# Kernel optimization log

Measured on AMD Instinct MI355X. Metric: run time of the kernel, lower is better.

The kernel has to match this reference:

```python
import jax, jax.numpy as jnp
import numpy as np

B = 8192          # graphs
A = 1024          # atoms per graph
F = 32            # max fragments per graph
N = B * A
VIRTUAL_IDX = 4   # HPARAMS.get_node_idx('ligand_virtual')


def setup_inputs() -> dict:
    key = jax.random.key(0)
    k1, k2, k3, k4 = jax.random.split(key, 4)
    pos = jax.random.normal(k1, (N, 3), dtype=jnp.float32) * 10.0
    # -1 marks non-ligand atoms (no fragment), as in frag_idx_map semantics
    frag_idx_map = jax.random.randint(k2, (N,), -1, F, dtype=jnp.int32)
    batch_idx = (jnp.arange(N, dtype=jnp.int32) // A).astype(jnp.int32)
    node_entity = jax.random.randint(k3, (N,), 0, 6, dtype=jnp.int32)
    mask = jax.random.bernoulli(k4, 0.95, (N,))
    return {"pos": pos, "frag_idx_map": frag_idx_map, "batch_idx": batch_idx,
            "node_entity": node_entity, "mask": mask,
            "num_graphs": B, "max_frags_per_graph": F}


def reference(pos, frag_idx_map, batch_idx, node_entity, mask,
              num_graphs, max_frags_per_graph):
    """Fused equivalent of get_flat_fragment_index + get_fragment_com.

    Returns (coms [B*F, 3], counts [B*F], flat_frag_idx [N]).
    Rows of coms beyond a graph's actual fragment count are zero-padded.
    """
    Bn = num_graphs
    Fm = max_frags_per_graph
    is_ligand = frag_idx_map >= 0

    # num_frags_per_graph[i] = max(frag_idx in graph i) + 1 (0 if none)
    fmax = jax.ops.segment_max(jnp.where(is_ligand, frag_idx_map, -1),
                               batch_idx, num_segments=Bn)
    nfrag = jnp.maximum(fmax, -1) + 1  # [B]
    offset = jnp.concatenate([jnp.zeros((1,), nfrag.dtype),
                              jnp.cumsum(nfrag)[:-1]])  # [B]

    # flat fragment index in [0, sum(F_i)), -1 for non-ligand atoms
    flat_frag_idx = jnp.where(is_ligand,
                              frag_idx_map + offset[batch_idx],
                              -1)

    # COM excludes virtual nodes and masked dummies
    valid = is_ligand & mask & (node_entity != VIRTUAL_IDX)
    n_seg = Bn * Fm
    seg = jnp.where(valid, flat_frag_idx, n_seg)  # dump invalid into trash segment
    w = valid.astype(pos.dtype)
    sums = jax.ops.segment_sum(pos * w[:, None], seg, num_segments=n_seg + 1)[:-1]
    cnt = jax.ops.segment_sum(w, seg, num_segments=n_seg + 1)[:-1]
    coms = sums / jnp.maximum(cnt, 1.0)[:, None]
    return coms, cnt, flat_frag_idx
```

## Files before the change

### kernel.cpp

```cpp
#include <hip/hip_runtime.h>

#define GA 1024
#define GF 32
#define VIRT 4

typedef _Float16 half8 __attribute__((ext_vector_type(8)));
typedef float f32x4 __attribute__((ext_vector_type(4)));
typedef unsigned int uint4v __attribute__((ext_vector_type(4)));

#define XSTRIDE 2080
#define KOFF    (4 * XSTRIDE)
#define FOFF    (KOFF + GA)
#define LDSSZ   (FOFF + 4 * GF * 4 * 4)

__device__ __forceinline__ unsigned int h2(float a, float b) {
    const unsigned short lo = __builtin_bit_cast(unsigned short, (_Float16)a);
    const unsigned short hi = __builtin_bit_cast(unsigned short, (_Float16)b);
    return (unsigned int)lo | ((unsigned int)hi << 16);
}

__global__ __launch_bounds__(256) void k_graph_acc(
    const float* __restrict__ pos,
    const int*   __restrict__ frag,
    const int*   __restrict__ entity,
    const int*   __restrict__ mask,
    float*       __restrict__ sums_cnt,
    int*         __restrict__ nfrag,
    unsigned*    __restrict__ frag8u)
{
    const int g    = blockIdx.x;
    const int t    = threadIdx.x;
    const int lane = t & 63;
    const int w    = t >> 6;

    __shared__ alignas(16) unsigned char lds[LDSSZ];
    __shared__ int s_wmax[4];

    const int i0 = g * GA + t * 4;
    const int4  f4 = *(const int4*)(frag   + i0);
    const int4  e4 = *(const int4*)(entity + i0);
    const int4  m4 = *(const int4*)(mask   + i0);
    const float4* p4 = (const float4*)(pos + (size_t)3 * i0);
    const float4 pa = p4[0], pb = p4[1], pc = p4[2];

    const unsigned s8p = (f4.x & 0xFFu)         | ((f4.y & 0xFFu) << 8)
                       | ((f4.z & 0xFFu) << 16) | ((unsigned)(f4.w & 0xFFu) << 24);
    frag8u[(size_t)g * (GA / 4) + t] = s8p;

    #define KEY(F,M,E) ((unsigned)(((F) >= 0 && (M) != 0 && (E) != VIRT) ? (unsigned)(F) : 0xFFu))
    const unsigned kp = KEY(f4.x,m4.x,e4.x)        | (KEY(f4.y,m4.y,e4.y) << 8)
                      | (KEY(f4.z,m4.z,e4.z) << 16) | (KEY(f4.w,m4.w,e4.w) << 24);
    *(unsigned*)(lds + KOFF + t * 4) = kp;
    #undef KEY

    *(uint2*)(lds + 0 * XSTRIDE + t * 8) = make_uint2(h2(pa.x, pa.w), h2(pb.z, pc.y));
    *(uint2*)(lds + 1 * XSTRIDE + t * 8) = make_uint2(h2(pa.y, pb.x), h2(pb.w, pc.z));
    *(uint2*)(lds + 2 * XSTRIDE + t * 8) = make_uint2(h2(pa.z, pb.y), h2(pc.x, pc.w));
    *(uint2*)(lds + 3 * XSTRIDE + t * 8) = make_uint2(0x3C003C00u, 0x3C003C00u);

    int lm = max(max(f4.x, f4.y), max(f4.z, f4.w));
    #pragma unroll
    for (int off = 32; off > 0; off >>= 1)
        lm = max(lm, __shfl_down(lm, off, 64));
    if (lane == 0) s_wmax[w] = lm;

    f32x4 acc0 = {0.f, 0.f, 0.f, 0.f};
    f32x4 acc1 = {0.f, 0.f, 0.f, 0.f};
    const int row = lane & 15;
    const int grp = lane >> 4;
    const unsigned xoff = (unsigned)((row & 3) * XSTRIDE + (w * 256 + grp * 8) * 2);
    const unsigned koff = (unsigned)(KOFF + w * 256 + grp * 8);

    #pragma unroll
    for (int s = 0; s < 8; ++s) {
        const uint2  kk = *(const uint2*)(lds + koff + s * 32);
        const uint4v bv = *(const uint4v*)(lds + xoff + s * 64);
        uint4v a0, a1;
        #pragma unroll
        for (int p = 0; p < 4; ++p) {
            const unsigned word = (p & 2) ? kk.y : kk.x;
            const unsigned k0 = (word >> ((p & 1) * 16)) & 0xFFu;
            const unsigned k1 = (word >> ((p & 1) * 16 + 8)) & 0xFFu;
            a0[p] = (k0 == (unsigned)row        ? 0x3C00u : 0u)
                  | (k1 == (unsigned)row        ? 0x3C000000u : 0u);
            a1[p] = (k0 == (unsigned)(row + 16) ? 0x3C00u : 0u)
                  | (k1 == (unsigned)(row + 16) ? 0x3C000000u : 0u);
        }
        acc0 = __builtin_amdgcn_mfma_f32_16x16x32_f16(
                   __builtin_bit_cast(half8, a0), __builtin_bit_cast(half8, bv), acc0, 0, 0, 0);
        acc1 = __builtin_amdgcn_mfma_f32_16x16x32_f16(
                   __builtin_bit_cast(half8, a1), __builtin_bit_cast(half8, bv), acc1, 0, 0, 0);
    }

    float* fold = (float*)(lds + FOFF);
    if (row < 4) {
        #pragma unroll
        for (int r = 0; r < 4; ++r) {
            fold[(w * GF + grp * 4 + r) * 4 + row]      = acc0[r];
            fold[(w * GF + 16 + grp * 4 + r) * 4 + row] = acc1[r];
        }
    }
    __syncthreads();
    if (t < GF * 4) {
        const float v = fold[t] + fold[128 + t] + fold[256 + t] + fold[384 + t];
        sums_cnt[(size_t)g * (GF * 4) + t] = v;
    }
    if (t == 0)
        nfrag[g] = max(max(s_wmax[0], s_wmax[1]), max(s_wmax[2], s_wmax[3])) + 1;
}

__global__ __launch_bounds__(256) void k_scan(
    const int* __restrict__ nfrag, int* __restrict__ offset, int B)
{
    const int t = threadIdx.x;
    const int C = B / 256;
    __shared__ int s[8192 + 256];
    __shared__ int ps[256];

    for (int k = 0; k < C; ++k) {
        const int idx = k * 256 + t;
        s[idx + (idx >> 5)] = nfrag[idx];
    }
    __syncthreads();

    int sum = 0;
    for (int k = 0; k < C; ++k) {
        const int idx = t * C + k;
        const int p = idx + (idx >> 5);
        const int v = s[p];
        s[p] = sum;
        sum += v;
    }
    ps[t] = sum;
    __syncthreads();

    for (int d = 1; d < 256; d <<= 1) {
        const int v = (t >= d) ? ps[t - d] : 0;
        __syncthreads();
        ps[t] += v;
        __syncthreads();
    }

    for (int k = 0; k < C; ++k) {
        const int idx = k * 256 + t;
        const int c = idx >> 5;
        const int pre = (c == 0) ? 0 : ps[c - 1];
        offset[idx] = pre + s[idx + (idx >> 5)];
    }
    if (t == 255) offset[B] = ps[255];
}

__global__ __launch_bounds__(256) void k_fin2(
    const int*      __restrict__ nfrag,
    const int*      __restrict__ offset,
    const float4*   __restrict__ sums_cnt,
    const unsigned* __restrict__ frag8u,
    float*          __restrict__ coms,
    float*          __restrict__ cnt_out,
    float4*         __restrict__ out4,
    int B)
{
    const int b = blockIdx.x;
    const int t = threadIdx.x;
    const int off = offset[b];

    {
        const float fo = (float)off;
        const unsigned kk = frag8u[(size_t)b * (GA / 4) + t];
        const int a0 = ((int)(kk << 24)) >> 24;
        const int a1 = ((int)(kk << 16)) >> 24;
        const int a2 = ((int)(kk <<  8)) >> 24;
        const int a3 = ((int)kk) >> 24;
        float4 o;
        o.x = (a0 >= 0) ? (float)a0 + fo : -1.0f;
        o.y = (a1 >= 0) ? (float)a1 + fo : -1.0f;
        o.z = (a2 >= 0) ? (float)a2 + fo : -1.0f;
        o.w = (a3 >= 0) ? (float)a3 + fo : -1.0f;
        out4[(size_t)b * (GA / 4) + t] = o;
    }

    if (t < GF) {
        if (t < nfrag[b]) {
            const float4 v = sums_cnt[(size_t)b * GF + t];
            const int rr = off + t;
            const float inv = 1.0f / fmaxf(v.w, 1.0f);
            coms[3 * rr + 0] = v.x * inv;
            coms[3 * rr + 1] = v.y * inv;
            coms[3 * rr + 2] = v.z * inv;
            cnt_out[rr] = v.w;
        }
        const int r = b * GF + t;
        if (r >= offset[B]) {
            coms[3 * r + 0] = 0.0f; coms[3 * r + 1] = 0.0f; coms[3 * r + 2] = 0.0f;
            cnt_out[r] = 0.0f;
        }
    }
}

extern "C" void kernel_launch(void* const* d_in, const int* in_sizes, int n_in,
                              void* d_out, int out_size, void* d_ws, size_t ws_size,
                              hipStream_t stream)
{
    const float* pos    = (const float*)d_in[0];
    const int*   frag   = (const int*)d_in[1];
    const int*   entity = (const int*)d_in[3];
    const int*   mask   = (const int*)d_in[4];

    const int N = in_sizes[1];
    const int B = N / GA;

    float*    sums_cnt = (float*)d_ws;
    int*      nfrag    = (int*)(sums_cnt + (size_t)B * GF * 4);
    int*      offset   = nfrag + B;
    unsigned* frag8u   = (unsigned*)(offset + B + 1);

    float* coms     = (float*)d_out;
    float* cnt_out  = coms + (size_t)B * GF * 3;
    float* flat_out = cnt_out + (size_t)B * GF;

    k_graph_acc<<<B, 256, 0, stream>>>(pos, frag, entity, mask,
                                       sums_cnt, nfrag, frag8u);

    k_scan<<<1, 256, 0, stream>>>(nfrag, offset, B);

    k_fin2<<<B, 256, 0, stream>>>(
        nfrag, offset, (const float4*)sums_cnt, (const unsigned*)frag8u,
        coms, cnt_out, (float4*)flat_out, B);
}
```

Measured before the change: 258.2 us.

## Split each graph across two 128-thread blocks and defer partial merges

```diff
diff --git a/kernel.cpp b/kernel.cpp
--- a/kernel.cpp
+++ b/kernel.cpp
@@ -8,10 +8,10 @@
 typedef float f32x4 __attribute__((ext_vector_type(4)));
 typedef unsigned int uint4v __attribute__((ext_vector_type(4)));
 
-#define XSTRIDE 2080
-#define KOFF    (4 * XSTRIDE)
-#define FOFF    (KOFF + GA)
-#define LDSSZ   (FOFF + 4 * GF * 4 * 4)
+#define XSTR2   1056
+#define KOFF2   (4 * XSTR2)
+#define FOFF2   (KOFF2 + 512)
+#define LDSSZ2  (FOFF2 + 1024)
 
 __device__ __forceinline__ unsigned int h2(float a, float b) {
     const unsigned short lo = __builtin_bit_cast(unsigned short, (_Float16)a);
@@ -19,62 +19,65 @@
     return (unsigned int)lo | ((unsigned int)hi << 16);
 }
 
-__global__ __launch_bounds__(256) void k_graph_acc(
+__global__ __launch_bounds__(128, 8) void k_graph_acc(
     const float* __restrict__ pos,
     const int*   __restrict__ frag,
     const int*   __restrict__ entity,
     const int*   __restrict__ mask,
-    float*       __restrict__ sums_cnt,
-    int*         __restrict__ nfrag,
+    float*       __restrict__ sums2,
+    int*         __restrict__ nfrag4,
     unsigned*    __restrict__ frag8u)
 {
-    const int g    = blockIdx.x;
+    const int bid  = blockIdx.x;
+    const int g    = bid >> 1;
+    const int half = bid & 1;
     const int t    = threadIdx.x;
     const int lane = t & 63;
     const int w    = t >> 6;
 
-    __shared__ alignas(16) unsigned char lds[LDSSZ];
-    __shared__ int s_wmax[4];
-
-    const int i0 = g * GA + t * 4;
-    const int4  f4 = *(const int4*)(frag   + i0);
-    const int4  e4 = *(const int4*)(entity + i0);
-    const int4  m4 = *(const int4*)(mask   + i0);
-    const float4* p4 = (const float4*)(pos + (size_t)3 * i0);
+    __shared__ alignas(16) unsigned char lds[LDSSZ2];
+
+    const int a0i = g * GA + half * 512 + t * 4;
+    const int4  f4 = *(const int4*)(frag   + a0i);
+    const int4  e4 = *(const int4*)(entity + a0i);
+    const int4  m4 = *(const int4*)(mask   + a0i);
+    const float4* p4 = (const float4*)(pos + (size_t)3 * a0i);
     const float4 pa = p4[0], pb = p4[1], pc = p4[2];
 
-    const unsigned s8p = (f4.x & 0xFFu)         | ((f4.y & 0xFFu) << 8)
-                       | ((f4.z & 0xFFu) << 16) | ((unsigned)(f4.w & 0xFFu) << 24);
-    frag8u[(size_t)g * (GA / 4) + t] = s8p;
+    if (frag8u) {
+        const unsigned s8p = (f4.x & 0xFFu)         | ((f4.y & 0xFFu) << 8)
+                           | ((f4.z & 0xFFu) << 16) | ((unsigned)(f4.w & 0xFFu) << 24);
+        frag8u[(size_t)g * 256 + half * 128 + t] = s8p;
+    }
 
     #define KEY(F,M,E) ((unsigned)(((F) >= 0 && (M) != 0 && (E) != VIRT) ? (unsigned)(F) : 0xFFu))
     const unsigned kp = KEY(f4.x,m4.x,e4.x)        | (KEY(f4.y,m4.y,e4.y) << 8)
                       | (KEY(f4.z,m4.z,e4.z) << 16) | (KEY(f4.w,m4.w,e4.w) << 24);
-    *(unsigned*)(lds + KOFF + t * 4) = kp;
+    *(unsigned*)(lds + KOFF2 + t * 4) = kp;
     #undef KEY
 
-    *(uint2*)(lds + 0 * XSTRIDE + t * 8) = make_uint2(h2(pa.x, pa.w), h2(pb.z, pc.y));
-    *(uint2*)(lds + 1 * XSTRIDE + t * 8) = make_uint2(h2(pa.y, pb.x), h2(pb.w, pc.z));
-    *(uint2*)(lds + 2 * XSTRIDE + t * 8) = make_uint2(h2(pa.z, pb.y), h2(pc.x, pc.w));
-    *(uint2*)(lds + 3 * XSTRIDE + t * 8) = make_uint2(0x3C003C00u, 0x3C003C00u);
+    *(uint2*)(lds + 0 * XSTR2 + t * 8) = make_uint2(h2(pa.x, pa.w), h2(pb.z, pc.y));
+    *(uint2*)(lds + 1 * XSTR2 + t * 8) = make_uint2(h2(pa.y, pb.x), h2(pb.w, pc.z));
+    *(uint2*)(lds + 2 * XSTR2 + t * 8) = make_uint2(h2(pa.z, pb.y), h2(pc.x, pc.w));
+    *(uint2*)(lds + 3 * XSTR2 + t * 8) = make_uint2(0x3C003C00u, 0x3C003C00u);
 
     int lm = max(max(f4.x, f4.y), max(f4.z, f4.w));
     #pragma unroll
     for (int off = 32; off > 0; off >>= 1)
         lm = max(lm, __shfl_down(lm, off, 64));
-    if (lane == 0) s_wmax[w] = lm;
+    if (lane == 0) nfrag4[g * 4 + half * 2 + w] = lm;
 
     f32x4 acc0 = {0.f, 0.f, 0.f, 0.f};
     f32x4 acc1 = {0.f, 0.f, 0.f, 0.f};
     const int row = lane & 15;
     const int grp = lane >> 4;
-    const unsigned xoff = (unsigned)((row & 3) * XSTRIDE + (w * 256 + grp * 8) * 2);
-    const unsigned koff = (unsigned)(KOFF + w * 256 + grp * 8);
+    const unsigned xo = (unsigned)((row & 3) * XSTR2 + (w * 256 + grp * 8) * 2);
+    const unsigned ko = (unsigned)(KOFF2 + w * 256 + grp * 8);
 
     #pragma unroll
     for (int s = 0; s < 8; ++s) {
-        const uint2  kk = *(const uint2*)(lds + koff + s * 32);
-        const uint4v bv = *(const uint4v*)(lds + xoff + s * 64);
+        const uint2  kk = *(const uint2*)(lds + ko + s * 32);
+        const uint4v bv = *(const uint4v*)(lds + xo + s * 64);
         uint4v a0, a1;
         #pragma unroll
         for (int p = 0; p < 4; ++p) {
@@ -92,25 +95,24 @@
                    __builtin_bit_cast(half8, a1), __builtin_bit_cast(half8, bv), acc1, 0, 0, 0);
     }
 
-    float* fold = (float*)(lds + FOFF);
+    float* fp = (float*)(lds + FOFF2 + w * 512);
     if (row < 4) {
         #pragma unroll
         for (int r = 0; r < 4; ++r) {
-            fold[(w * GF + grp * 4 + r) * 4 + row]      = acc0[r];
-            fold[(w * GF + 16 + grp * 4 + r) * 4 + row] = acc1[r];
+            fp[(grp * 4 + r) * 4 + row]      = acc0[r];
+            fp[(16 + grp * 4 + r) * 4 + row] = acc1[r];
         }
     }
     __syncthreads();
-    if (t < GF * 4) {
-        const float v = fold[t] + fold[128 + t] + fold[256 + t] + fold[384 + t];
-        sums_cnt[(size_t)g * (GF * 4) + t] = v;
-    }
-    if (t == 0)
-        nfrag[g] = max(max(s_wmax[0], s_wmax[1]), max(s_wmax[2], s_wmax[3])) + 1;
+    {
+        const float* f0 = (const float*)(lds + FOFF2);
+        const float v = f0[t] + f0[128 + t];
+        sums2[(size_t)(g * 2 + half) * 128 + t] = v;
+    }
 }
 
 __global__ __launch_bounds__(256) void k_scan(
-    const int* __restrict__ nfrag, int* __restrict__ offset, int B)
+    const int4* __restrict__ nfrag4v, int* __restrict__ offset, int B)
 {
     const int t = threadIdx.x;
     const int C = B / 256;
@@ -119,7 +121,8 @@
 
     for (int k = 0; k < C; ++k) {
         const int idx = k * 256 + t;
-        s[idx + (idx >> 5)] = nfrag[idx];
+        const int4 nv = nfrag4v[idx];
+        s[idx + (idx >> 5)] = max(max(nv.x, nv.y), max(nv.z, nv.w)) + 1;
     }
     __syncthreads();
 
@@ -151,10 +154,11 @@
 }
 
 __global__ __launch_bounds__(256) void k_fin2(
-    const int*      __restrict__ nfrag,
+    const int4*     __restrict__ nfrag4v,
     const int*      __restrict__ offset,
-    const float4*   __restrict__ sums_cnt,
+    const float4*   __restrict__ sums2v,
     const unsigned* __restrict__ frag8u,
+    const int4*     __restrict__ frag4,
     float*          __restrict__ coms,
     float*          __restrict__ cnt_out,
     float4*         __restrict__ out4,
@@ -166,22 +170,35 @@
 
     {
         const float fo = (float)off;
-        const unsigned kk = frag8u[(size_t)b * (GA / 4) + t];
-        const int a0 = ((int)(kk << 24)) >> 24;
-        const int a1 = ((int)(kk << 16)) >> 24;
-        const int a2 = ((int)(kk <<  8)) >> 24;
-        const int a3 = ((int)kk) >> 24;
         float4 o;
-        o.x = (a0 >= 0) ? (float)a0 + fo : -1.0f;
-        o.y = (a1 >= 0) ? (float)a1 + fo : -1.0f;
-        o.z = (a2 >= 0) ? (float)a2 + fo : -1.0f;
-        o.w = (a3 >= 0) ? (float)a3 + fo : -1.0f;
+        if (frag8u) {
+            const unsigned kk = frag8u[(size_t)b * (GA / 4) + t];
+            const int a0 = ((int)(kk << 24)) >> 24;
+            const int a1 = ((int)(kk << 16)) >> 24;
+            const int a2 = ((int)(kk <<  8)) >> 24;
+            const int a3 = ((int)kk) >> 24;
+            o.x = (a0 >= 0) ? (float)a0 + fo : -1.0f;
+            o.y = (a1 >= 0) ? (float)a1 + fo : -1.0f;
+            o.z = (a2 >= 0) ? (float)a2 + fo : -1.0f;
+            o.w = (a3 >= 0) ? (float)a3 + fo : -1.0f;
+        } else {
+            const int4 f = frag4[(size_t)b * (GA / 4) + t];
+            o.x = (f.x >= 0) ? (float)f.x + fo : -1.0f;
+            o.y = (f.y >= 0) ? (float)f.y + fo : -1.0f;
+            o.z = (f.z >= 0) ? (float)f.z + fo : -1.0f;
+            o.w = (f.w >= 0) ? (float)f.w + fo : -1.0f;
+        }
         out4[(size_t)b * (GA / 4) + t] = o;
     }
 
     if (t < GF) {
-        if (t < nfrag[b]) {
-            const float4 v = sums_cnt[(size_t)b * GF + t];
+        const int4 nv = nfrag4v[b];
+        const int nfr = max(max(nv.x, nv.y), max(nv.z, nv.w)) + 1;
+        if (t < nfr) {
+            const float4 va = sums2v[(size_t)(b * 2)     * GF + t];
+            const float4 vb = sums2v[(size_t)(b * 2 + 1) * GF + t];
+            const float4 v = make_float4(va.x + vb.x, va.y + vb.y,
+                                         va.z + vb.z, va.w + vb.w);
             const int rr = off + t;
             const float inv = 1.0f / fmaxf(v.w, 1.0f);
             coms[3 * rr + 0] = v.x * inv;
@@ -209,21 +226,25 @@
     const int N = in_sizes[1];
     const int B = N / GA;
 
-    float*    sums_cnt = (float*)d_ws;
-    int*      nfrag    = (int*)(sums_cnt + (size_t)B * GF * 4);
-    int*      offset   = nfrag + B;
-    unsigned* frag8u   = (unsigned*)(offset + B + 1);
+    float*    sums2  = (float*)d_ws;
+    int*      nfrag4 = (int*)(sums2 + (size_t)B * 2 * GF * 4);
+    int*      offset = nfrag4 + (size_t)B * 4;
+    unsigned* frag8u = (unsigned*)(offset + B + 1);
+    const size_t needed = (size_t)B * 2 * GF * 4 * 4 + (size_t)B * 16
+                        + (size_t)(B + 1) * 4 + (size_t)N;
+    if (ws_size < needed) frag8u = nullptr;
 
     float* coms     = (float*)d_out;
     float* cnt_out  = coms + (size_t)B * GF * 3;
     float* flat_out = cnt_out + (size_t)B * GF;
 
-    k_graph_acc<<<B, 256, 0, stream>>>(pos, frag, entity, mask,
-                                       sums_cnt, nfrag, frag8u);
-
-    k_scan<<<1, 256, 0, stream>>>(nfrag, offset, B);
+    k_graph_acc<<<2 * B, 128, 0, stream>>>(pos, frag, entity, mask,
+                                           sums2, nfrag4, frag8u);
+
+    k_scan<<<1, 256, 0, stream>>>((const int4*)nfrag4, offset, B);
 
     k_fin2<<<B, 256, 0, stream>>>(
-        nfrag, offset, (const float4*)sums_cnt, (const unsigned*)frag8u,
+        (const int4*)nfrag4, offset, (const float4*)sums2,
+        (const unsigned*)frag8u, (const int4*)frag,
         coms, cnt_out, (float4*)flat_out, B);
 }
```

Result: slower. 263.4 us (+2.0%).
